# Kernel optimization log

Measured on AMD Instinct MI355X. Metric: run time of the kernel, lower is better.

Reference implementation:

```python
import jax, jax.numpy as jnp
import numpy as np

B, L, E, D = 32, 1024, 512, 512  # batch, seq_len, input_size, per-direction hidden
SCALE = 1.4142135623730951  # rescale=True, highway_bias=0 -> sqrt(1+exp(0*2)) = sqrt(2)


def setup_inputs() -> dict:
    key = jax.random.key(0)
    ks = jax.random.split(key, 12)
    g = lambda k, shape, s: (jax.random.normal(k, shape, jnp.float32) * s)
    return {
        "seqs": jax.random.normal(ks[0], (B, L, E), jnp.float32),
        # layer 0: input E -> 2 dirs * 4 projections * D
        "W0": g(ks[1], (E, 8 * D), (1.0 / E) ** 0.5),
        "vf0": g(ks[2], (2, D), 0.1), "vr0": g(ks[3], (2, D), 0.1),
        "bf0": jnp.zeros((2, D), jnp.float32), "br0": jnp.zeros((2, D), jnp.float32),
        # layer 1: input 2D -> 2 dirs * 4 projections * D
        "W1": g(ks[4], (2 * D, 8 * D), (1.0 / (2 * D)) ** 0.5),
        "vf1": g(ks[5], (2, D), 0.1), "vr1": g(ks[6], (2, D), 0.1),
        "bf1": jnp.zeros((2, D), jnp.float32), "br1": jnp.zeros((2, D), jnp.float32),
        "lengths": jax.random.randint(ks[7], (B,), 1, L + 1, dtype=jnp.int32),
    }


def _sru_dir(u, vf, vr, bf, br, reverse):
    # u: (L, B, 4, D) -> h: (L, B, D), c_T: (B, D)
    def step(c, u_t):
        xt, fp, rp, xp = u_t[:, 0], u_t[:, 1], u_t[:, 2], u_t[:, 3]
        f = jax.nn.sigmoid(fp + vf * c + bf)
        c_new = f * c + (1.0 - f) * xt
        r = jax.nn.sigmoid(rp + vr * c + br)
        h = r * c_new + (1.0 - r) * xp * SCALE
        return c_new, h

    c0 = jnp.zeros((u.shape[1], u.shape[-1]), u.dtype)
    cT, hs = jax.lax.scan(step, c0, u, reverse=reverse)
    return hs, cT


def _sru_layer(x, W, vf, vr, bf, br):
    # x: (L, B, n_in)
    Lx, Bx = x.shape[0], x.shape[1]
    U = (x @ W).reshape(Lx, Bx, 2, 4, -1)  # dirs, (x_tilde, f, r, x_resid)
    h_f, c_f = _sru_dir(U[:, :, 0], vf[0], vr[0], bf[0], br[0], False)
    h_b, c_b = _sru_dir(U[:, :, 1], vf[1], vr[1], bf[1], br[1], True)
    return jnp.concatenate([h_f, h_b], -1), jnp.concatenate([c_f, c_b], -1)


def reference(seqs, W0, vf0, vr0, bf0, br0, W1, vf1, vr1, bf1, br1, lengths):
    x = jnp.transpose(seqs, (1, 0, 2))  # (L, B, E)
    out0, _ = _sru_layer(x, W0, vf0, vr0, bf0, br0)
    out1, c1 = _sru_layer(out0, W1, vf1, vr1, bf1, br1)
    # module returns (h[1], output.transpose(0,1)): layer-1 final cell state, (B,L,2D) outputs
    return c1, jnp.transpose(out1, (1, 0, 2))
```

## Files before the change

kernel.cpp:

```cpp
#include <hip/hip_runtime.h>
#include <cstdint>
#include <cstddef>

#define B_   32
#define L_   1024
#define D_   512
#define M_   (B_ * L_)
#define N8D  4096
#define SCALEF 1.4142135623730951f
#define LOG2E 1.4426950408889634f

typedef unsigned short u16;
typedef __bf16 bf16x8 __attribute__((ext_vector_type(8)));
typedef unsigned short u16x8 __attribute__((ext_vector_type(8)));
typedef unsigned short u16x4 __attribute__((ext_vector_type(4)));
typedef float f32x4 __attribute__((ext_vector_type(4)));

__device__ __forceinline__ float bf2f(u16 u) {
    union { unsigned int i; float f; } v; v.i = ((unsigned int)u) << 16; return v.f;
}
__device__ __forceinline__ u16 f2bf(float x) {
    union { float f; unsigned int i; } v; v.f = x;
    unsigned int r = (v.i + 0x7fffu + ((v.i >> 16) & 1u)) >> 16;
    return (u16)r;
}
__device__ __forceinline__ float sigmoid_fast(float z) {
    return __builtin_amdgcn_rcpf(1.0f + __builtin_amdgcn_exp2f(-LOG2E * z));
}

__device__ __forceinline__ void gl2lds16(const u16* g, u16* l) {
    __builtin_amdgcn_global_load_lds(
        (const __attribute__((address_space(1))) void*)g,
        (__attribute__((address_space(3))) void*)l, 16, 0, 0);
}

__global__ __launch_bounds__(256) void f32_to_bf16(const float* __restrict__ in,
                                                   u16* __restrict__ out) {
    size_t i = ((size_t)blockIdx.x * 256 + threadIdx.x) * 8;
    f32x4 v0 = *(const f32x4*)(in + i);
    f32x4 v1 = *(const f32x4*)(in + i + 4);
    u16x8 o;
#pragma unroll
    for (int q = 0; q < 4; ++q) { o[q] = f2bf(v0[q]); o[4 + q] = f2bf(v1[q]); }
    *(u16x8*)(out + i) = o;
}

__global__ __launch_bounds__(256) void transpose_w(const float* __restrict__ in,
                                                   u16* __restrict__ out,
                                                   int R, int C) {
    __shared__ u16 tile[32][33];
    int bx = blockIdx.x * 32;
    int by = blockIdx.y * 32;
    int tx = threadIdx.x & 31;
    int ty = threadIdx.x >> 5;
#pragma unroll
    for (int i = 0; i < 32; i += 8)
        tile[ty + i][tx] = f2bf(in[(size_t)(by + ty + i) * C + bx + tx]);
    __syncthreads();
#pragma unroll
    for (int i = 0; i < 32; i += 8) {
        int n = bx + ty + i;
        int p = (n >> 11) * 2048 + ((n & 511) << 2) + ((n >> 9) & 3);
        out[(size_t)p * R + by + tx] = tile[tx][ty + i];
    }
}

__global__ __launch_bounds__(256) void gemm_bt(const u16* __restrict__ A,
                                               const u16* __restrict__ BT,
                                               u16* __restrict__ U, int K) {
    __shared__ __align__(16) u16 As[128][32];
    __shared__ __align__(16) u16 Bs[128][32];
    const int t    = threadIdx.x;
    const int bn   = blockIdx.x * 128;
    const int bm   = blockIdx.y * 128;
    const int lane = t & 63;
    const int wave = t >> 6;
    const int wm   = (wave >> 1) * 64;
    const int wn   = (wave & 1) * 64;
    const int qm   = lane & 15;
    const int quad = lane >> 4;

    f32x4 acc[4][4];
#pragma unroll
    for (int i = 0; i < 4; ++i)
#pragma unroll
        for (int j = 0; j < 4; ++j)
            acc[i][j] = (f32x4)(0.0f);

    const int srow = t >> 2;
    const int c4   = t & 3;
    const int gcol = (c4 ^ ((srow >> 1) & 3)) * 8;
    const u16* ag = A  + (size_t)(bm + srow) * K + gcol;
    const u16* bg = BT + (size_t)(bn + srow) * K + gcol;
    u16* al = &As[srow][c4 * 8];
    u16* bl = &Bs[srow][c4 * 8];
    const size_t gstep = (size_t)64 * K;

    const int psw = (quad ^ ((qm >> 1) & 3)) * 8;

    for (int k0 = 0; k0 < K; k0 += 32) {
        __syncthreads();
        gl2lds16(ag + k0,         al);
        gl2lds16(ag + k0 + gstep, al + 64 * 32);
        gl2lds16(bg + k0,         bl);
        gl2lds16(bg + k0 + gstep, bl + 64 * 32);
        __syncthreads();

        bf16x8 a[4], b[4];
#pragma unroll
        for (int i = 0; i < 4; ++i)
            a[i] = *(const bf16x8*)(&As[wm + i * 16 + qm][psw]);
#pragma unroll
        for (int j = 0; j < 4; ++j)
            b[j] = *(const bf16x8*)(&Bs[wn + j * 16 + qm][psw]);
#pragma unroll
        for (int i = 0; i < 4; ++i)
#pragma unroll
            for (int j = 0; j < 4; ++j)
                acc[i][j] = __builtin_amdgcn_mfma_f32_16x16x32_bf16(a[i], b[j], acc[i][j], 0, 0, 0);
    }

#pragma unroll
    for (int i = 0; i < 4; ++i) {
        int row0 = bm + wm + i * 16 + quad * 4;
#pragma unroll
        for (int j = 0; j < 4; ++j) {
            int col = bn + wn + j * 16 + qm;
#pragma unroll
            for (int r = 0; r < 4; ++r)
                U[(size_t)(row0 + r) * N8D + col] = f2bf(acc[i][j][r]);
        }
    }
}

template<bool OUT_F32>
__global__ __launch_bounds__(256) void sru_scan(const u16* __restrict__ U,
                                                const float* __restrict__ vf,
                                                const float* __restrict__ vr,
                                                const float* __restrict__ bfv,
                                                const float* __restrict__ brv,
                                                void* __restrict__ Hv,
                                                void* __restrict__ Cv) {
    constexpr int PF = 32;
    constexpr int NB = L_ / PF;

    int gid = blockIdx.x * blockDim.x + threadIdx.x;
    int d   = gid & (D_ - 1);
    int dir = (gid >> 9) & 1;
    int b   = gid >> 10;
    int ch  = dir * D_ + d;

    const float vf_v = vf[ch];
    const float vr_v = vr[ch];
    const float bf_v = bfv[ch];
    const float br_v = brv[ch];

    const ptrdiff_t ustep = dir ? -(ptrdiff_t)N8D : (ptrdiff_t)N8D;
    const ptrdiff_t hstep = dir ? -(ptrdiff_t)1024 : (ptrdiff_t)1024;
    const u16* p0 = U + (size_t)b * L_ * N8D + dir * 2048 + d * 4
                      + (dir ? (size_t)(L_ - 1) * N8D : 0);
    const size_t hstart = (size_t)b * L_ * 1024 + ch + (dir ? (size_t)(L_ - 1) * 1024 : 0);
    float* Hf = (float*)Hv + hstart;
    u16*   Hh = (u16*)Hv + hstart;

    float c = 0.0f;

    auto loadB = [&](u16x4 (&buf)[PF], int tb) {
        const u16* base = p0 + (ptrdiff_t)tb * PF * ustep;
#pragma unroll
        for (int i = 0; i < PF; ++i)
            buf[i] = *(const u16x4*)(base + (ptrdiff_t)i * ustep);
    };
    auto compStore = [&](u16x4 (&buf)[PF], int tb) {
        const ptrdiff_t hb = (ptrdiff_t)tb * PF * hstep;
#pragma unroll
        for (int i = 0; i < PF; ++i) {
            float xt = bf2f(buf[i][0]), fp = bf2f(buf[i][1]);
            float rp = bf2f(buf[i][2]), xp = bf2f(buf[i][3]);
            float f = sigmoid_fast(fp + vf_v * c + bf_v);
            float r = sigmoid_fast(rp + vr_v * c + br_v);
            c = f * (c - xt) + xt;
            float xs = xp * SCALEF;
            float h  = r * (c - xs) + xs;
            ptrdiff_t ho = hb + (ptrdiff_t)i * hstep;
            if (OUT_F32) Hf[ho] = h; else Hh[ho] = f2bf(h);
        }
    };

    u16x4 b0[PF], b1[PF];
    loadB(b0, 0);
    loadB(b1, 1);
    for (int t = 0; t < NB; t += 2) {
        compStore(b0, t);
        if (t + 2 < NB) loadB(b0, t + 2);
        compStore(b1, t + 1);
        if (t + 3 < NB) loadB(b1, t + 3);
    }

    if (OUT_F32) ((float*)Cv)[b * 1024 + ch] = c;
    else         ((u16*)Cv)[b * 1024 + ch]  = f2bf(c);
}

extern "C" void kernel_launch(void* const* d_in, const int* in_sizes, int n_in,
                              void* d_out, int out_size, void* d_ws, size_t ws_size,
                              hipStream_t stream) {
    (void)in_sizes; (void)n_in; (void)out_size; (void)ws_size;

    const float* seqs = (const float*)d_in[0];
    const float* W0   = (const float*)d_in[1];
    const float* vf0  = (const float*)d_in[2];
    const float* vr0  = (const float*)d_in[3];
    const float* bf0  = (const float*)d_in[4];
    const float* br0  = (const float*)d_in[5];
    const float* W1   = (const float*)d_in[6];
    const float* vf1  = (const float*)d_in[7];
    const float* vr1  = (const float*)d_in[8];
    const float* bf1  = (const float*)d_in[9];
    const float* br1  = (const float*)d_in[10];

    float* out = (float*)d_out;
    char* ws = (char*)d_ws;

    const size_t U_BYTES  = (size_t)M_ * N8D * 2;
    const size_t H_BYTES  = (size_t)M_ * 1024 * 2;
    const size_t W0T_B    = (size_t)4096 * 512 * 2;
    const size_t W1T_B    = (size_t)4096 * 1024 * 2;

    u16* U   = (u16*)(ws);
    u16* H0  = (u16*)(ws + U_BYTES);
    u16* S16 = H0;
    u16* W0T = (u16*)(ws + U_BYTES + H_BYTES);
    u16* W1T = (u16*)(ws + U_BYTES + H_BYTES + W0T_B);
    u16* Cd  = (u16*)(ws + U_BYTES + H_BYTES + W0T_B + W1T_B);

    f32_to_bf16<<<dim3(M_ * 512 / 8 / 256), 256, 0, stream>>>(seqs, S16);

    transpose_w<<<dim3(4096 / 32, 512 / 32), 256, 0, stream>>>(W0, W0T, 512, 4096);
    transpose_w<<<dim3(4096 / 32, 1024 / 32), 256, 0, stream>>>(W1, W1T, 1024, 4096);

    gemm_bt<<<dim3(N8D / 128, M_ / 128), 256, 0, stream>>>(S16, W0T, U, 512);
    sru_scan<false><<<dim3(M_ / 256), 256, 0, stream>>>(U, vf0, vr0, bf0, br0, (void*)H0, (void*)Cd);

    gemm_bt<<<dim3(N8D / 128, M_ / 128), 256, 0, stream>>>(H0, W1T, U, 1024);
    sru_scan<true><<<dim3(M_ / 256), 256, 0, stream>>>(U, vf1, vr1, bf1, br1,
                                                       (void*)(out + B_ * 1024), (void*)out);
}
```

Before: 945.1 us.

## Replace 128x128 GEMM with double-buffered 256x256 pipelined MFMA GEMM

Replaces the GEMM kernel with a 512-thread, 256x256-tile kernel. It uses 128 KB of dynamic LDS and double-buffers the K slices, issuing asynchronous global-to-LDS loads that overlap with MFMA work through explicit barriers, waitcnts and setprio. It also adds an XOR-swizzled LDS layout and a workgroup index swizzle intended to improve L2 locality. The goal is higher MFMA utilisation and less exposed memory latency in both projection GEMMs. In exchange, register pressure and LDS use go up, occupancy drops, and the hand-ordered wait counts are fragile if they are wrong.

```diff
diff --git a/kernel.cpp b/kernel.cpp
--- a/kernel.cpp
+++ b/kernel.cpp
@@ -33,6 +33,8 @@
         (const __attribute__((address_space(1))) void*)g,
         (__attribute__((address_space(3))) void*)l, 16, 0, 0);
 }
+
+#define VMW(n) asm volatile("s_waitcnt vmcnt(" #n ")" ::: "memory")
 
 __global__ __launch_bounds__(256) void f32_to_bf16(const float* __restrict__ in,
                                                    u16* __restrict__ out) {
@@ -65,70 +67,122 @@
     }
 }
 
-__global__ __launch_bounds__(256) void gemm_bt(const u16* __restrict__ A,
+__global__ __launch_bounds__(512) void gemm256(const u16* __restrict__ A,
                                                const u16* __restrict__ BT,
                                                u16* __restrict__ U, int K) {
-    __shared__ __align__(16) u16 As[128][32];
-    __shared__ __align__(16) u16 Bs[128][32];
+    extern __shared__ __align__(16) u16 lds[];
     const int t    = threadIdx.x;
-    const int bn   = blockIdx.x * 128;
-    const int bm   = blockIdx.y * 128;
     const int lane = t & 63;
     const int wave = t >> 6;
-    const int wm   = (wave >> 1) * 64;
-    const int wn   = (wave & 1) * 64;
+    const int wm   = wave >> 2;
+    const int wn   = wave & 3;
     const int qm   = lane & 15;
     const int quad = lane >> 4;
 
-    f32x4 acc[4][4];
-#pragma unroll
-    for (int i = 0; i < 4; ++i)
-#pragma unroll
-        for (int j = 0; j < 4; ++j)
-            acc[i][j] = (f32x4)(0.0f);
-
-    const int srow = t >> 2;
-    const int c4   = t & 3;
-    const int gcol = (c4 ^ ((srow >> 1) & 3)) * 8;
-    const u16* ag = A  + (size_t)(bm + srow) * K + gcol;
-    const u16* bg = BT + (size_t)(bn + srow) * K + gcol;
-    u16* al = &As[srow][c4 * 8];
-    u16* bl = &Bs[srow][c4 * 8];
-    const size_t gstep = (size_t)64 * K;
-
-    const int psw = (quad ^ ((qm >> 1) & 3)) * 8;
-
-    for (int k0 = 0; k0 < K; k0 += 32) {
-        __syncthreads();
-        gl2lds16(ag + k0,         al);
-        gl2lds16(ag + k0 + gstep, al + 64 * 32);
-        gl2lds16(bg + k0,         bl);
-        gl2lds16(bg + k0 + gstep, bl + 64 * 32);
-        __syncthreads();
-
-        bf16x8 a[4], b[4];
-#pragma unroll
-        for (int i = 0; i < 4; ++i)
-            a[i] = *(const bf16x8*)(&As[wm + i * 16 + qm][psw]);
-#pragma unroll
-        for (int j = 0; j < 4; ++j)
-            b[j] = *(const bf16x8*)(&Bs[wn + j * 16 + qm][psw]);
-#pragma unroll
-        for (int i = 0; i < 4; ++i)
-#pragma unroll
-            for (int j = 0; j < 4; ++j)
-                acc[i][j] = __builtin_amdgcn_mfma_f32_16x16x32_bf16(a[i], b[j], acc[i][j], 0, 0, 0);
+    const int nwg = gridDim.x;
+    const int wg  = blockIdx.x;
+    const int swz = (wg & 7) * (nwg >> 3) + (wg >> 3);
+    const int bn  = (swz & 15) << 8;
+    const int bm  = (swz >> 4) << 8;
+
+    const int P0   = t * 16;
+    const int L0   = P0 ^ ((P0 >> 3) & 0x30);
+    const int srow = L0 >> 6;
+    const int scol = (L0 & 63) >> 1;
+    const u16* Ag = A  + (size_t)(bm + srow) * K + scol;
+    const u16* Bg = BT + (size_t)(bn + srow) * K + scol;
+    const size_t g128 = (size_t)128 * K;
+    u16* ldst = lds + t * 8;
+
+    const int fxor  = (quad * 16) ^ ((qm & 6) << 3);
+    const int aBase = (wm * 128 + qm) * 64 + fxor;
+    const int bBase = (wn * 64  + qm) * 64 + fxor;
+    const char* ldsc = (const char*)lds;
+
+    f32x4 acc[8][4];
+#pragma unroll
+    for (int i = 0; i < 8; ++i)
+#pragma unroll
+        for (int j = 0; j < 4; ++j) acc[i][j] = (f32x4)(0.0f);
+
+    bf16x8 bfr[4];
+
+#define STG(op, tile, ks, buf) do {                                          \
+        const u16* g_ = ((op) ? Bg : Ag) + (size_t)(tile) * 64 + (ks) * 32;  \
+        u16* l_ = ldst + (buf) * 32768 + (op) * 16384 + (ks) * 8192;         \
+        gl2lds16(g_, l_);                                                    \
+        gl2lds16(g_ + g128, l_ + 4096);                                      \
+    } while (0)
+
+#define PHASE(buf, mh, ks, STAGE_STMT, VM_STMT) do {                         \
+        const char* As_ = ldsc + ((buf) * 32768 + (ks) * 8192) * 2;          \
+        const char* Bs_ = ldsc + ((buf) * 32768 + 16384 + (ks) * 8192) * 2;  \
+        bf16x8 a_[4];                                                        \
+        _Pragma("unroll")                                                    \
+        for (int mi = 0; mi < 4; ++mi)                                       \
+            a_[mi] = *(const bf16x8*)(As_ + aBase + ((mh) * 64 + mi * 16) * 64); \
+        if ((mh) == 0) {                                                     \
+            _Pragma("unroll")                                                \
+            for (int nj = 0; nj < 4; ++nj)                                   \
+                bfr[nj] = *(const bf16x8*)(Bs_ + bBase + nj * 16 * 64);      \
+        }                                                                    \
+        STAGE_STMT;                                                          \
+        __builtin_amdgcn_s_barrier();                                        \
+        asm volatile("s_waitcnt lgkmcnt(0)" ::: "memory");                   \
+        __builtin_amdgcn_sched_barrier(0);                                   \
+        __builtin_amdgcn_s_setprio(1);                                       \
+        _Pragma("unroll")                                                    \
+        for (int mi = 0; mi < 4; ++mi)                                       \
+            _Pragma("unroll")                                                \
+            for (int nj = 0; nj < 4; ++nj)                                   \
+                acc[(mh) * 4 + mi][nj] = __builtin_amdgcn_mfma_f32_16x16x32_bf16( \
+                    a_[mi], bfr[nj], acc[(mh) * 4 + mi][nj], 0, 0, 0);       \
+        __builtin_amdgcn_s_setprio(0);                                       \
+        VM_STMT;                                                             \
+        __builtin_amdgcn_s_barrier();                                        \
+    } while (0)
+
+    const int nt = K >> 6;
+
+    STG(1, 0, 0, 0); STG(0, 0, 0, 0); STG(1, 0, 1, 0); STG(0, 0, 1, 0);
+    VMW(4);
+    STG(1, 1, 0, 1); STG(0, 1, 0, 1); STG(1, 1, 1, 1);
+    VMW(6);
+    __builtin_amdgcn_s_barrier();
+
+    const int niter = (nt >> 1) - 1;
+    for (int i = 0; i < niter; ++i) {
+        const int tp1 = 2 * i + 1, tp2 = 2 * i + 2, tp3 = 2 * i + 3;
+        PHASE(0, 0, 0, STG(0, tp1, 1, 1), );
+        PHASE(0, 1, 0, STG(1, tp2, 0, 0), );
+        PHASE(0, 0, 1, STG(0, tp2, 0, 0), );
+        PHASE(0, 1, 1, STG(1, tp2, 1, 0), VMW(6));
+        PHASE(1, 0, 0, STG(0, tp2, 1, 0), );
+        PHASE(1, 1, 0, STG(1, tp3, 0, 1), );
+        PHASE(1, 0, 1, STG(0, tp3, 0, 1), );
+        PHASE(1, 1, 1, STG(1, tp3, 1, 1), VMW(6));
     }
-
-#pragma unroll
-    for (int i = 0; i < 4; ++i) {
-        int row0 = bm + wm + i * 16 + quad * 4;
-#pragma unroll
-        for (int j = 0; j < 4; ++j) {
-            int col = bn + wn + j * 16 + qm;
+    PHASE(0, 0, 0, STG(0, nt - 1, 1, 1), );
+    PHASE(0, 1, 0, , );
+    PHASE(0, 0, 1, , );
+    PHASE(0, 1, 1, , VMW(4));
+    PHASE(1, 0, 0, , );
+    PHASE(1, 1, 0, , VMW(0));
+    PHASE(1, 0, 1, , );
+    PHASE(1, 1, 1, , );
+
+#undef PHASE
+#undef STG
+
+#pragma unroll
+    for (int i8 = 0; i8 < 8; ++i8) {
+        const int row0 = bm + wm * 128 + (i8 >> 2) * 64 + (i8 & 3) * 16 + quad * 4;
+#pragma unroll
+        for (int nj = 0; nj < 4; ++nj) {
+            const int col = bn + wn * 64 + nj * 16 + qm;
 #pragma unroll
             for (int r = 0; r < 4; ++r)
-                U[(size_t)(row0 + r) * N8D + col] = f2bf(acc[i][j][r]);
+                U[(size_t)(row0 + r) * N8D + col] = f2bf(acc[i8][nj][r]);
         }
     }
 }
@@ -238,10 +292,10 @@
     transpose_w<<<dim3(4096 / 32, 512 / 32), 256, 0, stream>>>(W0, W0T, 512, 4096);
     transpose_w<<<dim3(4096 / 32, 1024 / 32), 256, 0, stream>>>(W1, W1T, 1024, 4096);
 
-    gemm_bt<<<dim3(N8D / 128, M_ / 128), 256, 0, stream>>>(S16, W0T, U, 512);
+    gemm256<<<dim3(2048), 512, 131072, stream>>>(S16, W0T, U, 512);
     sru_scan<false><<<dim3(M_ / 256), 256, 0, stream>>>(U, vf0, vr0, bf0, br0, (void*)H0, (void*)Cd);
 
-    gemm_bt<<<dim3(N8D / 128, M_ / 128), 256, 0, stream>>>(H0, W1T, U, 1024);
+    gemm256<<<dim3(2048), 512, 131072, stream>>>(H0, W1T, U, 1024);
     sru_scan<true><<<dim3(M_ / 256), 256, 0, stream>>>(U, vf1, vr1, bf1, br1,
                                                        (void*)(out + B_ * 1024), (void*)out);
 }
```

Result: faster. 856.0 us (-9.4%).
